# Performance work log

Measured on AMD Instinct MI355X. Metric: run time of the kernel, lower is better.

Reference implementation:

```python
import jax, jax.numpy as jnp
import numpy as np

B, C, H, W = 2, 64, 224, 224
RC = 8            # channels // reduction
WS = 32           # window size
OV = 8            # overlap (= min(8, WS//4, H//4))
STRIDE = WS - OV  # 24
NH = (H + OV - 1) // STRIDE  # 9
NW = (W + OV - 1) // STRIDE  # 9
NT = WS * WS      # 1024 tokens per window


def setup_inputs() -> dict:
    key = jax.random.key(0)
    ks = jax.random.split(key, 8)
    sc = 1.0 / np.sqrt(C)
    return {
        "x": jax.random.normal(ks[0], (B, C, H, W), jnp.float32),
        "Wq": jax.random.normal(ks[1], (RC, C), jnp.float32) * sc,
        "bq": jax.random.normal(ks[2], (RC,), jnp.float32) * 0.01,
        "Wk": jax.random.normal(ks[3], (RC, C), jnp.float32) * sc,
        "bk": jax.random.normal(ks[4], (RC,), jnp.float32) * 0.01,
        "Wv": jax.random.normal(ks[5], (C, C), jnp.float32) * sc,
        "bv": jax.random.normal(ks[6], (C,), jnp.float32) * 0.01,
        "gamma": jnp.full((1,), 0.5, jnp.float32),
    }


def _forward(x, Wq, bq, Wk, bk, Wv, bv, gamma):
    # 1x1 convs on the full map (pointwise => commutes with windowing)
    q = jnp.einsum("oc,bchw->bohw", Wq, x) + bq[None, :, None, None]
    k = jnp.einsum("oc,bchw->bohw", Wk, x) + bk[None, :, None, None]
    v = jnp.einsum("oc,bchw->bohw", Wv, x) + bv[None, :, None, None]

    # window gather indices: [NH, WS], [NW, WS]
    hidx = STRIDE * jnp.arange(NH)[:, None] + jnp.arange(WS)[None, :]
    widx = STRIDE * jnp.arange(NW)[:, None] + jnp.arange(WS)[None, :]
    gi = hidx[:, None, :, None]   # [NH,1,WS,1]
    gj = widx[None, :, None, :]   # [1,NW,1,WS]

    def windows(t):  # [B,c,H,W] -> [B,NH,NW,c,NT]
        tw = t[:, :, gi, gj]                       # [B,c,NH,NW,WS,WS]
        tw = jnp.transpose(tw, (0, 2, 3, 1, 4, 5))  # [B,NH,NW,c,WS,WS]
        return tw.reshape(t.shape[0], NH, NW, t.shape[1], NT)

    qw, kw, vw = windows(q), windows(k), windows(v)

    # per-window attention: q tokens attend over k tokens
    attn = jnp.einsum("bijrp,bijrq->bijpq", qw, kw) / jnp.float32(np.sqrt(NT))
    attn = jax.nn.softmax(attn, axis=-1)
    ow = jnp.einsum("bijpq,bijcq->bijcp", attn, vw)      # [B,NH,NW,C,NT]
    ow = ow.reshape(B, NH, NW, C, WS, WS)
    ow = jnp.transpose(ow, (0, 3, 1, 2, 4, 5))            # [B,C,NH,NW,WS,WS]

    # fade weights (linspace 0..1 over OV rows/cols at interior window edges)
    fade = jnp.linspace(0.0, 1.0, OV, dtype=jnp.float32)
    rows = jnp.ones((NH, WS), jnp.float32)
    rows = rows.at[1:, :OV].multiply(fade)        # h_start > 0
    rows = rows.at[:-1, -OV:].multiply(fade[::-1])  # h_end < H
    cols = jnp.ones((NW, WS), jnp.float32)
    cols = cols.at[1:, :OV].multiply(fade)
    cols = cols.at[:-1, -OV:].multiply(fade[::-1])
    wgt = rows[:, None, :, None] * cols[None, :, None, :]  # [NH,NW,WS,WS]

    # overlap-add with blend weights
    out = jnp.zeros_like(x).at[:, :, gi, gj].add(wgt[None, None] * ow)
    cnt = jnp.zeros((H, W), jnp.float32).at[gi, gj].add(wgt)
    blended = out / (cnt[None, None] + 1e-8)
    return x + gamma[0] * blended


def reference(x, Wq, bq, Wk, bk, Wv, bv, gamma):
    return _forward(x, Wq, bq, Wk, bk, Wv, bv, gamma)
```

## Files before the change

### kernel.cpp

```cpp
#include <hip/hip_runtime.h>

#define Bn 2
#define Cn 64
#define Hn 224
#define Wn 224
#define HWn (Hn*Wn)
#define WSn 32
#define OVn 8
#define STRIDEn 24
#define NHn 9
#define NWn 9
#define NWT 28
#define VROW (NWT*Cn*8)
#define QSCALE (1.44269504088896f/32.0f)

typedef __bf16 bf16x8 __attribute__((ext_vector_type(8)));
typedef __bf16 bf16x4 __attribute__((ext_vector_type(4)));
typedef float f32x16 __attribute__((ext_vector_type(16)));
typedef unsigned int uint4v __attribute__((ext_vector_type(4)));

union PackU { uint4v u; bf16x8 h; };
union BfPair { __bf16 h[2]; unsigned u; };

__device__ __forceinline__ float fast_exp2(float x) {
#if __has_builtin(__builtin_amdgcn_exp2f)
  return __builtin_amdgcn_exp2f(x);
#else
  return exp2f(x);
#endif
}

__device__ __forceinline__ float fast_rcp(float x) {
#if __has_builtin(__builtin_amdgcn_rcpf)
  return __builtin_amdgcn_rcpf(x);
#else
  return 1.0f / x;
#endif
}

__device__ __forceinline__ float edge_w(int i, int p) {
  float w = 1.0f;
  if (i > 0 && p < OVn)            w *= (float)p * (1.0f/7.0f);
  if (i < NHn-1 && p >= WSn-OVn)   w *= (float)(WSn-1-p) * (1.0f/7.0f);
  return w;
}

__device__ __forceinline__ float covsum(int h) {
  int ihi = h / STRIDEn; if (ihi > NHn-1) ihi = NHn-1;
  float s = edge_w(ihi, h - STRIDEn*ihi);
  int ilo = ihi - 1;
  if (ilo >= 0) {
    int p = h - STRIDEn*ilo;
    if (p < WSn) s += edge_w(ilo, p);
  }
  return s;
}

__global__ __launch_bounds__(256) void qkv_kernel(
    const float* __restrict__ x,
    const float* __restrict__ Wq, const float* __restrict__ bq,
    const float* __restrict__ Wk, const float* __restrict__ bk,
    const float* __restrict__ Wv, const float* __restrict__ bv,
    __bf16* __restrict__ qb, __bf16* __restrict__ kb, __bf16* __restrict__ vb2)
{
  __shared__ __attribute__((aligned(16))) __bf16 sA[3][4][64][8];
  __shared__ float sBias[96];
  __shared__ float sT[4][32*17];

  int tid = threadIdx.x;
  for (int f = tid; f < 768; f += 256) {
    int t = f >> 8;
    int rem = f & 255;
    int s = rem >> 6;
    int ln = rem & 63;
    int row = t*32 + (ln & 31);
    int ch  = s*16 + (ln >> 5)*8;
    const float* src = nullptr;
    float scale = 1.0f;
    if (row < 8)       { src = Wq + row*64 + ch; scale = QSCALE; }
    else if (row < 16) { src = Wk + (row-8)*64 + ch; }
    else if (row < 80) { src = Wv + (row-16)*64 + ch; }
    bf16x8 a = {};
    if (src) {
      #pragma unroll
      for (int j = 0; j < 8; ++j) a[j] = (__bf16)(src[j] * scale);
    }
    *(bf16x8*)&sA[t][s][ln][0] = a;
  }
  if (tid < 96) {
    float bb = 0.f;
    if (tid < 8)       bb = bq[tid] * QSCALE;
    else if (tid < 16) bb = bk[tid-8];
    else if (tid < 80) bb = bv[tid-16];
    sBias[tid] = bb;
  }
  __syncthreads();

  int widx = tid >> 6;
  int lane = tid & 63;
  int lo = lane & 31, hi = lane >> 5;
  int gid = blockIdx.x*4 + widx;
  int wg  = gid % 7;
  int rem = gid / 7;
  int h = rem % Hn;
  int b = rem / Hn;
  int w0 = wg * 32;
  const float* xb = x + (size_t)b*Cn*HWn + (size_t)h*Wn + w0 + lo;

  f32x16 d0 = {}, d1 = {}, d2 = {};
  #pragma unroll
  for (int s = 0; s < 4; ++s) {
    bf16x8 bfr;
    #pragma unroll
    for (int j = 0; j < 8; ++j)
      bfr[j] = (__bf16)xb[(size_t)(s*16 + 8*hi + j)*HWn];
    bf16x8 a0 = *(const bf16x8*)&sA[0][s][lane][0];
    bf16x8 a1 = *(const bf16x8*)&sA[1][s][lane][0];
    bf16x8 a2 = *(const bf16x8*)&sA[2][s][lane][0];
    d0 = __builtin_amdgcn_mfma_f32_32x32x16_bf16(a0, bfr, d0, 0, 0, 0);
    d1 = __builtin_amdgcn_mfma_f32_32x32x16_bf16(a1, bfr, d1, 0, 0, 0);
    d2 = __builtin_amdgcn_mfma_f32_32x32x16_bf16(a2, bfr, d2, 0, 0, 0);
  }

  float* T = sT[widx];
  #pragma unroll
  for (int r = 0; r < 8; ++r) {
    int row = (r&3) + 8*(r>>2) + 4*hi;
    T[lo*17 + row] = d0[r] + sBias[row];
  }
  __syncthreads();
  PackU o;
  #pragma unroll
  for (int m = 0; m < 8; ++m) o.h[m] = (__bf16)T[lo*17 + hi*8 + m];
  size_t pix = (size_t)(b*Hn + h)*Wn + w0 + lo;
  if (hi == 0) *(uint4v*)(qb + pix*8) = o.u;
  else         *(uint4v*)(kb + pix*8) = o.u;

  __bf16* vbl = vb2 + ((size_t)(b*Hn + h)*NWT + (w0>>3))*(Cn*8)
                + (size_t)(lo>>3)*(Cn*8) + (lo&7);
  #pragma unroll
  for (int r = 8; r < 16; ++r) {
    int row = (r&3) + 8*(r>>2) + 4*hi;
    vbl[(size_t)(row-16)*8] = (__bf16)(d0[r] + sBias[row]);
  }
  #pragma unroll
  for (int r = 0; r < 16; ++r) {
    int row = 32 + (r&3) + 8*(r>>2) + 4*hi;
    vbl[(size_t)(row-16)*8] = (__bf16)(d1[r] + sBias[row]);
  }
  #pragma unroll
  for (int r = 0; r < 8; ++r) {
    int row = 64 + (r&3) + 8*(r>>2) + 4*hi;
    vbl[(size_t)(row-16)*8] = (__bf16)(d2[r] + sBias[row]);
  }
}

__global__ __launch_bounds__(256, 4) void attn_kernel(
    const __bf16* __restrict__ qb, const __bf16* __restrict__ kb,
    const __bf16* __restrict__ vb2, __bf16* __restrict__ ob2)
{
  __shared__ float LB[4*1056];

  int bid = blockIdx.x;
  int bidm = (bid & 7) * 162 + (bid >> 3);
  int win = bidm >> 3;
  int rg  = bidm & 7;
  int b  = win / (NHn*NWn);
  int ij = win - b*(NHn*NWn);
  int wi = ij / NWn;
  int wj = ij - wi*NWn;

  int tid  = threadIdx.x;
  int widx = tid >> 6;
  int lane = tid & 63;
  int ph = rg*4 + widx;
  int lo = lane & 31, hi = lane >> 5;
  int h0 = wi*STRIDEn, w0 = wj*STRIDEn;

  bf16x8 qf = *(const bf16x8*)(qb + ((size_t)(b*Hn + h0 + ph)*Wn + w0 + lo) * 8);
  if (hi) qf = (bf16x8){};

  const __bf16* kbase = kb + ((size_t)(b*Hn + h0)*Wn + w0 + lo) * 8;
  const __bf16* vbase = vb2 + (((size_t)(b*Hn + h0)*NWT + (w0>>3))*Cn + lo)*8
                        + (size_t)hi*512;

  f32x16 acc0 = {}, acc1 = {};
  float ls[4] = {0.f, 0.f, 0.f, 0.f};

  #pragma unroll 4
  for (int kt = 0; kt < 32; ++kt) {
    bf16x8 kf = *(const bf16x8*)(kbase + (size_t)kt*Wn*8);

    const __bf16* vk = vbase + (size_t)kt*VROW;
    bf16x8 vf00 = *(const bf16x8*)(vk);
    bf16x8 vf01 = *(const bf16x8*)(vk + 256);
    bf16x8 vf10 = *(const bf16x8*)(vk + 1024);
    bf16x8 vf11 = *(const bf16x8*)(vk + 1280);

    f32x16 s = __builtin_amdgcn_mfma_f32_32x32x16_bf16(kf, qf, (f32x16){}, 0, 0, 0);

    unsigned w[8];
    #pragma unroll
    for (int d = 0; d < 8; ++d) {
      float a  = fast_exp2(s[2*d]);
      float b2 = fast_exp2(s[2*d+1]);
      ls[d & 3] += a + b2;
      BfPair pr; pr.h[0] = (__bf16)a; pr.h[1] = (__bf16)b2;
      w[d] = pr.u;
    }
    auto s02 = __builtin_amdgcn_permlane32_swap((int)w[0], (int)w[2], false, false);
    auto s13 = __builtin_amdgcn_permlane32_swap((int)w[1], (int)w[3], false, false);
    auto s46 = __builtin_amdgcn_permlane32_swap((int)w[4], (int)w[6], false, false);
    auto s57 = __builtin_amdgcn_permlane32_swap((int)w[5], (int)w[7], false, false);

    PackU pa0, pa1;
    pa0.u = (uint4v){(unsigned)s02[0], (unsigned)s13[0], (unsigned)s02[1], (unsigned)s13[1]};
    pa1.u = (uint4v){(unsigned)s46[0], (unsigned)s57[0], (unsigned)s46[1], (unsigned)s57[1]};

    __builtin_amdgcn_s_setprio(1);
    acc0 = __builtin_amdgcn_mfma_f32_32x32x16_bf16(pa0.h, vf00, acc0, 0, 0, 0);
    acc1 = __builtin_amdgcn_mfma_f32_32x32x16_bf16(pa0.h, vf01, acc1, 0, 0, 0);
    acc0 = __builtin_amdgcn_mfma_f32_32x32x16_bf16(pa1.h, vf10, acc0, 0, 0, 0);
    acc1 = __builtin_amdgcn_mfma_f32_32x32x16_bf16(pa1.h, vf11, acc1, 0, 0, 0);
    __builtin_amdgcn_s_setprio(0);
  }

  float lsum = (ls[0] + ls[1]) + (ls[2] + ls[3]);
  lsum += __shfl_xor(lsum, 32);
  float sc = edge_w(wi, ph) * edge_w(wj, lo) * fast_rcp(lsum);

  float* T = LB + (size_t)widx*1056;
  __bf16* ob = ob2 + ((size_t)win*64)*1024 + ph*32;

  #pragma unroll
  for (int r = 0; r < 16; ++r) {
    int qc = (r&3) + 8*(r>>2) + 4*hi;
    T[qc*33 + lo] = acc0[r];
  }
  #pragma unroll
  for (int rr = 0; rr < 16; ++rr) {
    int c0 = 2*rr + hi;
    ob[(size_t)c0*1024 + lo] = (__bf16)(T[lo*33 + c0] * sc);
  }
  #pragma unroll
  for (int r = 0; r < 16; ++r) {
    int qc = (r&3) + 8*(r>>2) + 4*hi;
    T[qc*33 + lo] = acc1[r];
  }
  #pragma unroll
  for (int rr = 0; rr < 16; ++rr) {
    int c0 = 2*rr + hi;
    ob[(size_t)(32 + c0)*1024 + lo] = (__bf16)(T[lo*33 + c0] * sc);
  }
}

__global__ __launch_bounds__(256) void final_kernel(
    const float* __restrict__ x, const float* __restrict__ gamma,
    const __bf16* __restrict__ ob2, float* __restrict__ out)
{
  int idx4 = blockIdx.x * 256 + threadIdx.x;
  int w4    = idx4 % (Wn/4);
  int rowid = idx4 / (Wn/4);
  int h  = rowid % Hn;
  int cb = rowid / Hn;
  int c  = cb & 63;
  int b  = cb >> 6;
  int w0 = w4*4;

  int ihi = h  / STRIDEn; if (ihi > NHn-1) ihi = NHn-1;
  int jhi = w0 / STRIDEn; if (jhi > NWn-1) jhi = NWn-1;

  float s0 = 0.f, s1 = 0.f, s2 = 0.f, s3 = 0.f;
  #pragma unroll
  for (int dy = 0; dy < 2; ++dy) {
    int wi = ihi - dy;
    if (wi < 0) continue;
    int ph = h - STRIDEn*wi;
    if (ph >= WSn) continue;
    #pragma unroll
    for (int dx = 0; dx < 2; ++dx) {
      int wj = jhi - dx;
      if (wj < 0) continue;
      int pw = w0 - STRIDEn*wj;
      if (pw >= WSn) continue;
      const __bf16* src = ob2 + (((size_t)(b*81 + wi*9 + wj)*64 + c) << 10) + ph*WSn + pw;
      bf16x4 v = *(const bf16x4*)src;
      s0 += (float)v[0]; s1 += (float)v[1]; s2 += (float)v[2]; s3 += (float)v[3];
    }
  }

  float g = gamma[0];
  float rs = covsum(h);
  float i0 = fast_rcp(rs * covsum(w0+0) + 1e-8f);
  float i1 = fast_rcp(rs * covsum(w0+1) + 1e-8f);
  float i2 = fast_rcp(rs * covsum(w0+2) + 1e-8f);
  float i3 = fast_rcp(rs * covsum(w0+3) + 1e-8f);
  float4 xv = ((const float4*)x)[idx4];
  float4 r;
  r.x = xv.x + g * s0 * i0;
  r.y = xv.y + g * s1 * i1;
  r.z = xv.z + g * s2 * i2;
  r.w = xv.w + g * s3 * i3;
  ((float4*)out)[idx4] = r;
}

extern "C" void kernel_launch(void* const* d_in, const int* in_sizes, int n_in,
                              void* d_out, int out_size, void* d_ws, size_t ws_size,
                              hipStream_t stream) {
  const float* x     = (const float*)d_in[0];
  const float* Wq    = (const float*)d_in[1];
  const float* bq    = (const float*)d_in[2];
  const float* Wk    = (const float*)d_in[3];
  const float* bk    = (const float*)d_in[4];
  const float* Wv    = (const float*)d_in[5];
  const float* bv    = (const float*)d_in[6];
  const float* gamma = (const float*)d_in[7];
  float* out = (float*)d_out;

  __bf16* qb  = (__bf16*)d_ws;
  __bf16* kb  = qb  + (size_t)Bn*HWn*8;
  __bf16* vb2 = kb  + (size_t)Bn*HWn*8;
  __bf16* ob2 = vb2 + (size_t)Bn*Cn*HWn;

  qkv_kernel<<<784, 256, 0, stream>>>(x, Wq, bq, Wk, bk, Wv, bv, qb, kb, vb2);
  attn_kernel<<<Bn*NHn*NWn*8, 256, 0, stream>>>(qb, kb, vb2, ob2);
  final_kernel<<<(Bn*Cn*HWn/4)/256, 256, 0, stream>>>(x, gamma, ob2, out);
}
```

Before: 80.27 us.

## Software-pipeline QK MFMA ahead of softmax-PV with dual accumulators

Restructures the key-tile loop so the QK^T MFMA for the next tile is issued before the exp/softmax and PV MFMAs of the current tile. Two independent accumulator sets are used for even and odd tiles and summed at the end. This is meant to overlap the matrix unit with the VALU exp work and to break the accumulator dependency chain. It doubles the accumulator registers, and the launch bound drops from 4 to 2 waves per SIMD, which lowers occupancy.

```diff
diff --git a/kernel.cpp b/kernel.cpp
--- a/kernel.cpp
+++ b/kernel.cpp
@@ -155,7 +155,45 @@
   }
 }
 
-__global__ __launch_bounds__(256, 4) void attn_kernel(
+__device__ __forceinline__ f32x16 qk_tile(const __bf16* kbase, int kt, bf16x8 qf) {
+  bf16x8 kf = *(const bf16x8*)(kbase + (size_t)kt*Wn*8);
+  return __builtin_amdgcn_mfma_f32_32x32x16_bf16(kf, qf, (f32x16){}, 0, 0, 0);
+}
+
+__device__ __forceinline__ void softmax_pv(const f32x16& s, const __bf16* vk,
+                                           f32x16& a0, f32x16& a1, float* ls) {
+  bf16x8 vf00 = *(const bf16x8*)(vk);
+  bf16x8 vf01 = *(const bf16x8*)(vk + 256);
+  bf16x8 vf10 = *(const bf16x8*)(vk + 1024);
+  bf16x8 vf11 = *(const bf16x8*)(vk + 1280);
+
+  unsigned w[8];
+  #pragma unroll
+  for (int d = 0; d < 8; ++d) {
+    float a  = fast_exp2(s[2*d]);
+    float b2 = fast_exp2(s[2*d+1]);
+    ls[d & 3] += a + b2;
+    BfPair pr; pr.h[0] = (__bf16)a; pr.h[1] = (__bf16)b2;
+    w[d] = pr.u;
+  }
+  auto s02 = __builtin_amdgcn_permlane32_swap((int)w[0], (int)w[2], false, false);
+  auto s13 = __builtin_amdgcn_permlane32_swap((int)w[1], (int)w[3], false, false);
+  auto s46 = __builtin_amdgcn_permlane32_swap((int)w[4], (int)w[6], false, false);
+  auto s57 = __builtin_amdgcn_permlane32_swap((int)w[5], (int)w[7], false, false);
+
+  PackU pa0, pa1;
+  pa0.u = (uint4v){(unsigned)s02[0], (unsigned)s13[0], (unsigned)s02[1], (unsigned)s13[1]};
+  pa1.u = (uint4v){(unsigned)s46[0], (unsigned)s57[0], (unsigned)s46[1], (unsigned)s57[1]};
+
+  __builtin_amdgcn_s_setprio(1);
+  a0 = __builtin_amdgcn_mfma_f32_32x32x16_bf16(pa0.h, vf00, a0, 0, 0, 0);
+  a1 = __builtin_amdgcn_mfma_f32_32x32x16_bf16(pa0.h, vf01, a1, 0, 0, 0);
+  a0 = __builtin_amdgcn_mfma_f32_32x32x16_bf16(pa1.h, vf10, a0, 0, 0, 0);
+  a1 = __builtin_amdgcn_mfma_f32_32x32x16_bf16(pa1.h, vf11, a1, 0, 0, 0);
+  __builtin_amdgcn_s_setprio(0);
+}
+
+__global__ __launch_bounds__(256, 2) void attn_kernel(
     const __bf16* __restrict__ qb, const __bf16* __restrict__ kb,
     const __bf16* __restrict__ vb2, __bf16* __restrict__ ob2)
 {
@@ -184,45 +222,24 @@
   const __bf16* vbase = vb2 + (((size_t)(b*Hn + h0)*NWT + (w0>>3))*Cn + lo)*8
                         + (size_t)hi*512;
 
-  f32x16 acc0 = {}, acc1 = {};
+  f32x16 accA0 = {}, accA1 = {}, accB0 = {}, accB1 = {};
   float ls[4] = {0.f, 0.f, 0.f, 0.f};
 
-  #pragma unroll 4
-  for (int kt = 0; kt < 32; ++kt) {
-    bf16x8 kf = *(const bf16x8*)(kbase + (size_t)kt*Wn*8);
-
-    const __bf16* vk = vbase + (size_t)kt*VROW;
-    bf16x8 vf00 = *(const bf16x8*)(vk);
-    bf16x8 vf01 = *(const bf16x8*)(vk + 256);
-    bf16x8 vf10 = *(const bf16x8*)(vk + 1024);
-    bf16x8 vf11 = *(const bf16x8*)(vk + 1280);
-
-    f32x16 s = __builtin_amdgcn_mfma_f32_32x32x16_bf16(kf, qf, (f32x16){}, 0, 0, 0);
-
-    unsigned w[8];
-    #pragma unroll
-    for (int d = 0; d < 8; ++d) {
-      float a  = fast_exp2(s[2*d]);
-      float b2 = fast_exp2(s[2*d+1]);
-      ls[d & 3] += a + b2;
-      BfPair pr; pr.h[0] = (__bf16)a; pr.h[1] = (__bf16)b2;
-      w[d] = pr.u;
-    }
-    auto s02 = __builtin_amdgcn_permlane32_swap((int)w[0], (int)w[2], false, false);
-    auto s13 = __builtin_amdgcn_permlane32_swap((int)w[1], (int)w[3], false, false);
-    auto s46 = __builtin_amdgcn_permlane32_swap((int)w[4], (int)w[6], false, false);
-    auto s57 = __builtin_amdgcn_permlane32_swap((int)w[5], (int)w[7], false, false);
-
-    PackU pa0, pa1;
-    pa0.u = (uint4v){(unsigned)s02[0], (unsigned)s13[0], (unsigned)s02[1], (unsigned)s13[1]};
-    pa1.u = (uint4v){(unsigned)s46[0], (unsigned)s57[0], (unsigned)s46[1], (unsigned)s57[1]};
-
-    __builtin_amdgcn_s_setprio(1);
-    acc0 = __builtin_amdgcn_mfma_f32_32x32x16_bf16(pa0.h, vf00, acc0, 0, 0, 0);
-    acc1 = __builtin_amdgcn_mfma_f32_32x32x16_bf16(pa0.h, vf01, acc1, 0, 0, 0);
-    acc0 = __builtin_amdgcn_mfma_f32_32x32x16_bf16(pa1.h, vf10, acc0, 0, 0, 0);
-    acc1 = __builtin_amdgcn_mfma_f32_32x32x16_bf16(pa1.h, vf11, acc1, 0, 0, 0);
-    __builtin_amdgcn_s_setprio(0);
+  f32x16 sA = qk_tile(kbase, 0, qf);
+  f32x16 sB;
+  #pragma unroll 2
+  for (int kt2 = 0; kt2 < 16; ++kt2) {
+    sB = qk_tile(kbase, 2*kt2 + 1, qf);
+    softmax_pv(sA, vbase + (size_t)(2*kt2)*VROW, accA0, accA1, ls);
+    if (kt2 < 15) sA = qk_tile(kbase, 2*kt2 + 2, qf);
+    softmax_pv(sB, vbase + (size_t)(2*kt2 + 1)*VROW, accB0, accB1, ls);
+  }
+
+  f32x16 acc0, acc1;
+  #pragma unroll
+  for (int r = 0; r < 16; ++r) {
+    acc0[r] = accA0[r] + accB0[r];
+    acc1[r] = accA1[r] + accB1[r];
   }
 
   float lsum = (ls[0] + ls[1]) + (ls[2] + ls[3]);
```

Result: slower. 83.69 us (+4.3%).

## Process two query rows per wavefront to reuse K/V loads

Applied to the files above, without the earlier changes.

Each wavefront now handles two query rows of a window instead of one, sharing each K and V fragment load across both rows' score and PV MFMAs. The grid is halved and launch bounds drop to 2 blocks per CU to make room for the doubled accumulators. The aim is to halve global K/V traffic per unit of work. The cost is higher register pressure and lower occupancy, which may reduce latency hiding.

```diff
diff --git a/kernel.cpp b/kernel.cpp
--- a/kernel.cpp
+++ b/kernel.cpp
@@ -155,16 +155,43 @@
   }
 }
 
-__global__ __launch_bounds__(256, 4) void attn_kernel(
+__device__ __forceinline__ void softmax_pv2(
+    const f32x16& s, bf16x8 vf00, bf16x8 vf01, bf16x8 vf10, bf16x8 vf11,
+    f32x16& a0, f32x16& a1, float* ls) {
+  unsigned w[8];
+  #pragma unroll
+  for (int d = 0; d < 8; ++d) {
+    float a  = fast_exp2(s[2*d]);
+    float b2 = fast_exp2(s[2*d+1]);
+    ls[d & 3] += a + b2;
+    BfPair pr; pr.h[0] = (__bf16)a; pr.h[1] = (__bf16)b2;
+    w[d] = pr.u;
+  }
+  auto s02 = __builtin_amdgcn_permlane32_swap((int)w[0], (int)w[2], false, false);
+  auto s13 = __builtin_amdgcn_permlane32_swap((int)w[1], (int)w[3], false, false);
+  auto s46 = __builtin_amdgcn_permlane32_swap((int)w[4], (int)w[6], false, false);
+  auto s57 = __builtin_amdgcn_permlane32_swap((int)w[5], (int)w[7], false, false);
+  PackU pa0, pa1;
+  pa0.u = (uint4v){(unsigned)s02[0], (unsigned)s13[0], (unsigned)s02[1], (unsigned)s13[1]};
+  pa1.u = (uint4v){(unsigned)s46[0], (unsigned)s57[0], (unsigned)s46[1], (unsigned)s57[1]};
+  __builtin_amdgcn_s_setprio(1);
+  a0 = __builtin_amdgcn_mfma_f32_32x32x16_bf16(pa0.h, vf00, a0, 0, 0, 0);
+  a1 = __builtin_amdgcn_mfma_f32_32x32x16_bf16(pa0.h, vf01, a1, 0, 0, 0);
+  a0 = __builtin_amdgcn_mfma_f32_32x32x16_bf16(pa1.h, vf10, a0, 0, 0, 0);
+  a1 = __builtin_amdgcn_mfma_f32_32x32x16_bf16(pa1.h, vf11, a1, 0, 0, 0);
+  __builtin_amdgcn_s_setprio(0);
+}
+
+__global__ __launch_bounds__(256, 2) void attn_kernel(
     const __bf16* __restrict__ qb, const __bf16* __restrict__ kb,
     const __bf16* __restrict__ vb2, __bf16* __restrict__ ob2)
 {
   __shared__ float LB[4*1056];
 
   int bid = blockIdx.x;
-  int bidm = (bid & 7) * 162 + (bid >> 3);
-  int win = bidm >> 3;
-  int rg  = bidm & 7;
+  int bidm = (bid & 7) * 81 + (bid >> 3);
+  int win  = bidm >> 2;
+  int quad = bidm & 3;
   int b  = win / (NHn*NWn);
   int ij = win - b*(NHn*NWn);
   int wi = ij / NWn;
@@ -173,85 +200,71 @@
   int tid  = threadIdx.x;
   int widx = tid >> 6;
   int lane = tid & 63;
-  int ph = rg*4 + widx;
+  int rp   = quad*4 + widx;
+  int ph0 = 2*rp, ph1 = 2*rp + 1;
   int lo = lane & 31, hi = lane >> 5;
   int h0 = wi*STRIDEn, w0 = wj*STRIDEn;
 
-  bf16x8 qf = *(const bf16x8*)(qb + ((size_t)(b*Hn + h0 + ph)*Wn + w0 + lo) * 8);
-  if (hi) qf = (bf16x8){};
+  bf16x8 qf0 = *(const bf16x8*)(qb + ((size_t)(b*Hn + h0 + ph0)*Wn + w0 + lo) * 8);
+  bf16x8 qf1 = *(const bf16x8*)(qb + ((size_t)(b*Hn + h0 + ph1)*Wn + w0 + lo) * 8);
+  if (hi) { qf0 = (bf16x8){}; qf1 = (bf16x8){}; }
 
   const __bf16* kbase = kb + ((size_t)(b*Hn + h0)*Wn + w0 + lo) * 8;
   const __bf16* vbase = vb2 + (((size_t)(b*Hn + h0)*NWT + (w0>>3))*Cn + lo)*8
                         + (size_t)hi*512;
 
-  f32x16 acc0 = {}, acc1 = {};
-  float ls[4] = {0.f, 0.f, 0.f, 0.f};
-
-  #pragma unroll 4
+  f32x16 acc00 = {}, acc01 = {}, acc10 = {}, acc11 = {};
+  float ls0[4] = {0.f, 0.f, 0.f, 0.f};
+  float ls1[4] = {0.f, 0.f, 0.f, 0.f};
+
+  #pragma unroll 2
   for (int kt = 0; kt < 32; ++kt) {
     bf16x8 kf = *(const bf16x8*)(kbase + (size_t)kt*Wn*8);
-
     const __bf16* vk = vbase + (size_t)kt*VROW;
     bf16x8 vf00 = *(const bf16x8*)(vk);
     bf16x8 vf01 = *(const bf16x8*)(vk + 256);
     bf16x8 vf10 = *(const bf16x8*)(vk + 1024);
     bf16x8 vf11 = *(const bf16x8*)(vk + 1280);
 
-    f32x16 s = __builtin_amdgcn_mfma_f32_32x32x16_bf16(kf, qf, (f32x16){}, 0, 0, 0);
-
-    unsigned w[8];
-    #pragma unroll
-    for (int d = 0; d < 8; ++d) {
-      float a  = fast_exp2(s[2*d]);
-      float b2 = fast_exp2(s[2*d+1]);
-      ls[d & 3] += a + b2;
-      BfPair pr; pr.h[0] = (__bf16)a; pr.h[1] = (__bf16)b2;
-      w[d] = pr.u;
-    }
-    auto s02 = __builtin_amdgcn_permlane32_swap((int)w[0], (int)w[2], false, false);
-    auto s13 = __builtin_amdgcn_permlane32_swap((int)w[1], (int)w[3], false, false);
-    auto s46 = __builtin_amdgcn_permlane32_swap((int)w[4], (int)w[6], false, false);
-    auto s57 = __builtin_amdgcn_permlane32_swap((int)w[5], (int)w[7], false, false);
-
-    PackU pa0, pa1;
-    pa0.u = (uint4v){(unsigned)s02[0], (unsigned)s13[0], (unsigned)s02[1], (unsigned)s13[1]};
-    pa1.u = (uint4v){(unsigned)s46[0], (unsigned)s57[0], (unsigned)s46[1], (unsigned)s57[1]};
-
-    __builtin_amdgcn_s_setprio(1);
-    acc0 = __builtin_amdgcn_mfma_f32_32x32x16_bf16(pa0.h, vf00, acc0, 0, 0, 0);
-    acc1 = __builtin_amdgcn_mfma_f32_32x32x16_bf16(pa0.h, vf01, acc1, 0, 0, 0);
-    acc0 = __builtin_amdgcn_mfma_f32_32x32x16_bf16(pa1.h, vf10, acc0, 0, 0, 0);
-    acc1 = __builtin_amdgcn_mfma_f32_32x32x16_bf16(pa1.h, vf11, acc1, 0, 0, 0);
-    __builtin_amdgcn_s_setprio(0);
-  }
-
-  float lsum = (ls[0] + ls[1]) + (ls[2] + ls[3]);
-  lsum += __shfl_xor(lsum, 32);
-  float sc = edge_w(wi, ph) * edge_w(wj, lo) * fast_rcp(lsum);
+    f32x16 s0 = __builtin_amdgcn_mfma_f32_32x32x16_bf16(kf, qf0, (f32x16){}, 0, 0, 0);
+    f32x16 s1 = __builtin_amdgcn_mfma_f32_32x32x16_bf16(kf, qf1, (f32x16){}, 0, 0, 0);
+
+    softmax_pv2(s0, vf00, vf01, vf10, vf11, acc00, acc01, ls0);
+    softmax_pv2(s1, vf00, vf01, vf10, vf11, acc10, acc11, ls1);
+  }
+
+  float lsum0 = (ls0[0] + ls0[1]) + (ls0[2] + ls0[3]);
+  float lsum1 = (ls1[0] + ls1[1]) + (ls1[2] + ls1[3]);
+  lsum0 += __shfl_xor(lsum0, 32);
+  lsum1 += __shfl_xor(lsum1, 32);
+  float ewj = edge_w(wj, lo);
+  float sc0 = edge_w(wi, ph0) * ewj * fast_rcp(lsum0);
+  float sc1 = edge_w(wi, ph1) * ewj * fast_rcp(lsum1);
 
   float* T = LB + (size_t)widx*1056;
-  __bf16* ob = ob2 + ((size_t)win*64)*1024 + ph*32;
-
-  #pragma unroll
-  for (int r = 0; r < 16; ++r) {
-    int qc = (r&3) + 8*(r>>2) + 4*hi;
-    T[qc*33 + lo] = acc0[r];
-  }
-  #pragma unroll
-  for (int rr = 0; rr < 16; ++rr) {
-    int c0 = 2*rr + hi;
-    ob[(size_t)c0*1024 + lo] = (__bf16)(T[lo*33 + c0] * sc);
-  }
-  #pragma unroll
-  for (int r = 0; r < 16; ++r) {
-    int qc = (r&3) + 8*(r>>2) + 4*hi;
-    T[qc*33 + lo] = acc1[r];
-  }
-  #pragma unroll
-  for (int rr = 0; rr < 16; ++rr) {
-    int c0 = 2*rr + hi;
-    ob[(size_t)(32 + c0)*1024 + lo] = (__bf16)(T[lo*33 + c0] * sc);
-  }
+  __bf16* ob0 = ob2 + ((size_t)win*64)*1024 + ph0*32;
+  __bf16* ob1 = ob2 + ((size_t)win*64)*1024 + ph1*32;
+
+  #pragma unroll
+  for (int r = 0; r < 16; ++r) { int qc = (r&3)+8*(r>>2)+4*hi; T[qc*33+lo] = acc00[r]; }
+  #pragma unroll
+  for (int rr = 0; rr < 16; ++rr) { int c0 = 2*rr+hi;
+    ob0[(size_t)c0*1024 + lo] = (__bf16)(T[lo*33 + c0] * sc0); }
+  #pragma unroll
+  for (int r = 0; r < 16; ++r) { int qc = (r&3)+8*(r>>2)+4*hi; T[qc*33+lo] = acc01[r]; }
+  #pragma unroll
+  for (int rr = 0; rr < 16; ++rr) { int c0 = 2*rr+hi;
+    ob0[(size_t)(32 + c0)*1024 + lo] = (__bf16)(T[lo*33 + c0] * sc0); }
+  #pragma unroll
+  for (int r = 0; r < 16; ++r) { int qc = (r&3)+8*(r>>2)+4*hi; T[qc*33+lo] = acc10[r]; }
+  #pragma unroll
+  for (int rr = 0; rr < 16; ++rr) { int c0 = 2*rr+hi;
+    ob1[(size_t)c0*1024 + lo] = (__bf16)(T[lo*33 + c0] * sc1); }
+  #pragma unroll
+  for (int r = 0; r < 16; ++r) { int qc = (r&3)+8*(r>>2)+4*hi; T[qc*33+lo] = acc11[r]; }
+  #pragma unroll
+  for (int rr = 0; rr < 16; ++rr) { int c0 = 2*rr+hi;
+    ob1[(size_t)(32 + c0)*1024 + lo] = (__bf16)(T[lo*33 + c0] * sc1); }
 }
 
 __global__ __launch_bounds__(256) void final_kernel(
@@ -323,6 +336,6 @@
   __bf16* ob2 = vb2 + (size_t)Bn*Cn*HWn;
 
   qkv_kernel<<<784, 256, 0, stream>>>(x, Wq, bq, Wk, bk, Wv, bv, qb, kb, vb2);
-  attn_kernel<<<Bn*NHn*NWn*8, 256, 0, stream>>>(qb, kb, vb2, ob2);
+  attn_kernel<<<Bn*NHn*NWn*4, 256, 0, stream>>>(qb, kb, vb2, ob2);
   final_kernel<<<(Bn*Cn*HWn/4)/256, 256, 0, stream>>>(x, gamma, ob2, out);
 }
```

Measured after the change: 81.81 us. Within noise of the previous version (+1.9%).
